# Kernel optimization log

Measured on AMD Instinct MI355X. Metric: run time of the kernel, lower is better.

Reference implementation:

```python
import jax, jax.numpy as jnp
import numpy as np

TEMPERATURE = 0.05
EPS = 1e-8  # torch.cosine_similarity eps


def setup_inputs() -> dict:
    key = jax.random.key(0)
    k1, k2 = jax.random.split(key)
    N, D = 8192, 256
    text_embeddings = jax.random.normal(k1, (N, D), dtype=jnp.float32)
    text_pos_embeddings = jax.random.normal(k2, (N, D), dtype=jnp.float32)
    return {"text_embeddings": text_embeddings, "text_pos_embeddings": text_pos_embeddings}


def reference(text_embeddings, text_pos_embeddings):
    # cosine similarity via normalize + single GEMM (same math as broadcasted
    # torch.cosine_similarity, which clamps norms at eps)
    a_norm = jnp.maximum(jnp.linalg.norm(text_embeddings, axis=-1, keepdims=True), EPS)
    b_norm = jnp.maximum(jnp.linalg.norm(text_pos_embeddings, axis=-1, keepdims=True), EPS)
    a = text_embeddings / a_norm  # [N, D]
    b = text_pos_embeddings / b_norm  # [N, D]
    sim = jnp.einsum("nd,md->nm", a, b) / TEMPERATURE  # [N, N]
    # cross-entropy with labels = arange(N): mean over rows of -log_softmax diag
    logp = jax.nn.log_softmax(sim, axis=-1)
    loss = -jnp.mean(jnp.diagonal(logp))
    return loss
```

## Files before the change

### kernel.cpp

```cpp
#include <hip/hip_runtime.h>
#include <hip/hip_bf16.h>
#include <math.h>

#define DIM 256

typedef float f32x4 __attribute__((ext_vector_type(4)));
typedef int   i32x8 __attribute__((ext_vector_type(8)));

__constant__ const float kTempInvLog2e = 20.0f * 1.4426950408889634f;
#define LN2 0.6931471805599453f
#define EPS_NORM 1e-8f
#define SCALE_ONE 0x7F7F7F7Fu

static __device__ inline unsigned f2fp8x4(float4 v, float s) {
    int r = 0;
    r = __builtin_amdgcn_cvt_pk_fp8_f32(v.x * s, v.y * s, r, false);
    r = __builtin_amdgcn_cvt_pk_fp8_f32(v.z * s, v.w * s, r, true);
    return (unsigned)r;
}

static __device__ inline i32x8 ld_frag32(const void* p0, const void* p1) {
    uint4 a = *(const uint4*)p0;
    uint4 b = *(const uint4*)p1;
    i32x8 v;
    v[0] = a.x; v[1] = a.y; v[2] = a.z; v[3] = a.w;
    v[4] = b.x; v[5] = b.y; v[6] = b.z; v[7] = b.w;
    return v;
}

__global__ __launch_bounds__(256) void normpack_kernel(
    const float* __restrict__ A, const float* __restrict__ B,
    unsigned char* __restrict__ Apk, unsigned char* __restrict__ Bpk,
    float* __restrict__ diag, float* __restrict__ rowsum,
    unsigned* __restrict__ counter, int n)
{
    __shared__ uint4 lA[256];
    __shared__ uint4 lB[256];
    const int t = threadIdx.x;
    const int rl = t >> 4;
    const int c16 = t & 15;
    const int r = blockIdx.x * 16 + rl;

    if (blockIdx.x == 0 && t == 0) counter[0] = 0;

    const float4* pa = (const float4*)(A + (size_t)r * DIM + c16 * 16);
    const float4* pb = (const float4*)(B + (size_t)r * DIM + c16 * 16);
    float4 a0 = pa[0], a1 = pa[1], a2 = pa[2], a3 = pa[3];
    float4 b0 = pb[0], b1 = pb[1], b2 = pb[2], b3 = pb[3];

    float ssa = a0.x*a0.x + a0.y*a0.y + a0.z*a0.z + a0.w*a0.w
              + a1.x*a1.x + a1.y*a1.y + a1.z*a1.z + a1.w*a1.w
              + a2.x*a2.x + a2.y*a2.y + a2.z*a2.z + a2.w*a2.w
              + a3.x*a3.x + a3.y*a3.y + a3.z*a3.z + a3.w*a3.w;
    float ssb = b0.x*b0.x + b0.y*b0.y + b0.z*b0.z + b0.w*b0.w
              + b1.x*b1.x + b1.y*b1.y + b1.z*b1.z + b1.w*b1.w
              + b2.x*b2.x + b2.y*b2.y + b2.z*b2.z + b2.w*b2.w
              + b3.x*b3.x + b3.y*b3.y + b3.z*b3.z + b3.w*b3.w;
    float dd  = a0.x*b0.x + a0.y*b0.y + a0.z*b0.z + a0.w*b0.w
              + a1.x*b1.x + a1.y*b1.y + a1.z*b1.z + a1.w*b1.w
              + a2.x*b2.x + a2.y*b2.y + a2.z*b2.z + a2.w*b2.w
              + a3.x*b3.x + a3.y*b3.y + a3.z*b3.z + a3.w*b3.w;
#pragma unroll
    for (int m = 1; m < 16; m <<= 1) {
        ssa += __shfl_xor(ssa, m, 64);
        ssb += __shfl_xor(ssb, m, 64);
        dd  += __shfl_xor(dd, m, 64);
    }
    float na = fmaxf(sqrtf(ssa), EPS_NORM);
    float nb = fmaxf(sqrtf(ssb), EPS_NORM);
    float sa = kTempInvLog2e / na;
    float sb = 1.0f / nb;
    if (c16 == 0) {
        diag[r] = dd / (na * nb) * kTempInvLog2e;
        rowsum[r] = 0.0f;
    }

    const int u = ((c16 >> 3) << 7) + ((c16 & 1) << 6) + rl + ((c16 & 7) >> 1) * 16;
    uint4 ga, gb;
    ga.x = f2fp8x4(a0, sa); ga.y = f2fp8x4(a1, sa);
    ga.z = f2fp8x4(a2, sa); ga.w = f2fp8x4(a3, sa);
    gb.x = f2fp8x4(b0, sb); gb.y = f2fp8x4(b1, sb);
    gb.z = f2fp8x4(b2, sb); gb.w = f2fp8x4(b3, sb);
    lA[u] = ga; lB[u] = gb;
    __syncthreads();

    ((uint4*)Apk)[(size_t)blockIdx.x * 256 + t] = lA[t];
    ((uint4*)Bpk)[(size_t)blockIdx.x * 256 + t] = lB[t];
}

static __device__ inline void async_copy16(const void* g, void* l) {
    __builtin_amdgcn_global_load_lds(
        (const __attribute__((address_space(1))) unsigned int*)g,
        (__attribute__((address_space(3))) unsigned int*)l, 16, 0, 0);
}

__global__ __launch_bounds__(256, 2) void gemm_lse_kernel(
    const unsigned char* __restrict__ Apk, const unsigned char* __restrict__ Bpk,
    float* __restrict__ rowsum, const float* __restrict__ diag,
    unsigned* __restrict__ counter, float* __restrict__ out, int n)
{
    __shared__ char ldsbuf[16384];
    const int t = threadIdx.x;
    const int lane = t & 63;
    const int w = t >> 6;
    const int c = lane & 15;
    const int q = lane >> 4;

    const int i = blockIdx.x;
    const int split = ((i & 7) << 1) | ((i >> 3) & 1);
    const int rowblk = i >> 4;
    const int rowbase = rowblk * 256 + w * 64;

    i32x8 afrag[4][2];
#pragma unroll
    for (int m = 0; m < 4; ++m) {
        const int AT = rowblk * 16 + w * 4 + m;
#pragma unroll
        for (int kc = 0; kc < 2; ++kc) {
            const char* base = (const char*)Apk + ((size_t)AT * 2 + kc) * 2048 + lane * 16;
            afrag[m][kc] = ld_frag32(base, base + 1024);
        }
    }
#pragma unroll
    for (int m = 0; m < 4; ++m)
#pragma unroll
        for (int kc = 0; kc < 2; ++kc)
            asm volatile("" : "+v"(afrag[m][kc]));

    float sums[16];
#pragma unroll
    for (int s = 0; s < 16; ++s) sums[s] = 0.0f;

    const char* bbase = (const char*)Bpk + (size_t)split * 32 * 4096;
    const int niter = 16;

    {
        const char* src = bbase + w * 2048 + (size_t)lane * 16;
        char* dst = ldsbuf + w * 2048;
        async_copy16(src, dst);
        async_copy16(src + 1024, dst + 1024);
    }
    __syncthreads();

    for (int it = 0; it < niter; ++it) {
        const int cur = it & 1;
        if (it + 1 < niter) {
            const char* src = bbase + (size_t)(it + 1) * 8192 + w * 2048 + (size_t)lane * 16;
            char* dst = ldsbuf + (cur ^ 1) * 8192 + w * 2048;
            async_copy16(src, dst);
            async_copy16(src + 1024, dst + 1024);
        }

        f32x4 acc[4][2];
#pragma unroll
        for (int m = 0; m < 4; ++m)
#pragma unroll
            for (int nc = 0; nc < 2; ++nc)
                acc[m][nc] = (f32x4){0.f, 0.f, 0.f, 0.f};

        const char* lb = ldsbuf + cur * 8192 + (size_t)lane * 16;
#pragma unroll
        for (int nc = 0; nc < 2; ++nc) {
#pragma unroll
            for (int kc = 0; kc < 2; ++kc) {
                const char* p = lb + nc * 4096 + kc * 2048;
                i32x8 bfrag = ld_frag32(p, p + 1024);
#pragma unroll
                for (int m = 0; m < 4; ++m)
                    acc[m][nc] = __builtin_amdgcn_mfma_scale_f32_16x16x128_f8f6f4(
                        afrag[m][kc], bfrag, acc[m][nc],
                        0, 0,
                        0, SCALE_ONE,
                        0, SCALE_ONE);
            }
        }

#pragma unroll
        for (int m = 0; m < 4; ++m)
#pragma unroll
            for (int nc = 0; nc < 2; ++nc)
#pragma unroll
                for (int r = 0; r < 4; ++r)
                    sums[m * 4 + r] += __builtin_amdgcn_exp2f(acc[m][nc][r]);

        __syncthreads();
    }

#pragma unroll
    for (int s = 0; s < 16; ++s) {
        float v = sums[s];
        v += __shfl_xor(v, 1, 64);
        v += __shfl_xor(v, 2, 64);
        v += __shfl_xor(v, 4, 64);
        v += __shfl_xor(v, 8, 64);
        sums[s] = v;
    }
    if (c == 0) {
#pragma unroll
        for (int m = 0; m < 4; ++m)
#pragma unroll
            for (int r = 0; r < 4; ++r)
                atomicAdd(&rowsum[rowbase + m * 16 + q * 4 + r], sums[m * 4 + r]);
    }

    __syncthreads();
    __shared__ unsigned lastFlag;
    if (t == 0) {
        __threadfence();
        lastFlag = (__hip_atomic_fetch_add(counter, 1u, __ATOMIC_ACQ_REL,
                                           __HIP_MEMORY_SCOPE_AGENT)
                    == gridDim.x - 1) ? 1u : 0u;
    }
    __syncthreads();
    if (lastFlag) {
        float local = 0.0f;
        for (int row = t; row < n; row += 256) {
            float rs = __hip_atomic_load(&rowsum[row], __ATOMIC_RELAXED,
                                         __HIP_MEMORY_SCOPE_AGENT);
            local += log2f(rs) - diag[row];
        }
#pragma unroll
        for (int m = 1; m < 64; m <<= 1)
            local += __shfl_xor(local, m, 64);
        float* red = (float*)ldsbuf;
        if ((t & 63) == 0) red[t >> 6] = local;
        __syncthreads();
        if (t == 0) out[0] = (red[0] + red[1] + red[2] + red[3]) * (LN2 / (float)n);
    }
}

extern "C" void kernel_launch(void* const* d_in, const int* in_sizes, int n_in,
                              void* d_out, int out_size, void* d_ws, size_t ws_size,
                              hipStream_t stream) {
    const int n = in_sizes[0] / DIM;
    const float* A = (const float*)d_in[0];
    const float* B = (const float*)d_in[1];
    float* out = (float*)d_out;

    unsigned char* Apk = (unsigned char*)d_ws;
    unsigned char* Bpk = Apk + (size_t)n * DIM;
    float* rowsum = (float*)(Bpk + (size_t)n * DIM);
    float* diag = rowsum + n;
    unsigned* counter = (unsigned*)(diag + n);

    normpack_kernel<<<n / 16, 256, 0, stream>>>(A, B, Apk, Bpk, diag, rowsum, counter, n);

    gemm_lse_kernel<<<(n / 256) * 16, 256, 0, stream>>>(Apk, Bpk, rowsum, diag, counter, out, n);
}
```

Measured before the change: 108.4 us.

## Load B fragments directly from global into registers with register double-buffering

Drops the LDS staging of B tiles (async global_load_lds plus per-iteration __syncthreads) and instead has each wave load its B fragments straight from global memory into two register buffers, ping-ponged across a fully unrolled loop. Each wave now reads the whole B tile itself instead of sharing one LDS copy across the block's four waves. This removes the block-wide barriers and LDS round-trips, but raises global/L2 traffic and register pressure, which may affect occupancy at 2 blocks per CU.

Result: no change. 108.0 us (-0.4%).

```diff
diff --git a/kernel.cpp b/kernel.cpp
--- a/kernel.cpp
+++ b/kernel.cpp
@@ -1,5 +1,4 @@
 #include <hip/hip_runtime.h>
-#include <hip/hip_bf16.h>
 #include <math.h>
 
 #define DIM 256
@@ -19,9 +18,7 @@
     return (unsigned)r;
 }
 
-static __device__ inline i32x8 ld_frag32(const void* p0, const void* p1) {
-    uint4 a = *(const uint4*)p0;
-    uint4 b = *(const uint4*)p1;
+static __device__ inline i32x8 mk_frag(uint4 a, uint4 b) {
     i32x8 v;
     v[0] = a.x; v[1] = a.y; v[2] = a.z; v[3] = a.w;
     v[4] = b.x; v[5] = b.y; v[6] = b.z; v[7] = b.w;
@@ -88,18 +85,11 @@
     ((uint4*)Bpk)[(size_t)blockIdx.x * 256 + t] = lB[t];
 }
 
-static __device__ inline void async_copy16(const void* g, void* l) {
-    __builtin_amdgcn_global_load_lds(
-        (const __attribute__((address_space(1))) unsigned int*)g,
-        (__attribute__((address_space(3))) unsigned int*)l, 16, 0, 0);
-}
-
 __global__ __launch_bounds__(256, 2) void gemm_lse_kernel(
     const unsigned char* __restrict__ Apk, const unsigned char* __restrict__ Bpk,
     float* __restrict__ rowsum, const float* __restrict__ diag,
     unsigned* __restrict__ counter, float* __restrict__ out, int n)
 {
-    __shared__ char ldsbuf[16384];
     const int t = threadIdx.x;
     const int lane = t & 63;
     const int w = t >> 6;
@@ -118,7 +108,7 @@
 #pragma unroll
         for (int kc = 0; kc < 2; ++kc) {
             const char* base = (const char*)Apk + ((size_t)AT * 2 + kc) * 2048 + lane * 16;
-            afrag[m][kc] = ld_frag32(base, base + 1024);
+            afrag[m][kc] = mk_frag(*(const uint4*)base, *(const uint4*)(base + 1024));
         }
     }
 #pragma unroll
@@ -131,60 +121,43 @@
 #pragma unroll
     for (int s = 0; s < 16; ++s) sums[s] = 0.0f;
 
-    const char* bbase = (const char*)Bpk + (size_t)split * 32 * 4096;
-    const int niter = 16;
-
-    {
-        const char* src = bbase + w * 2048 + (size_t)lane * 16;
-        char* dst = ldsbuf + w * 2048;
-        async_copy16(src, dst);
-        async_copy16(src + 1024, dst + 1024);
-    }
-    __syncthreads();
-
-    for (int it = 0; it < niter; ++it) {
-        const int cur = it & 1;
-        if (it + 1 < niter) {
-            const char* src = bbase + (size_t)(it + 1) * 8192 + w * 2048 + (size_t)lane * 16;
-            char* dst = ldsbuf + (cur ^ 1) * 8192 + w * 2048;
-            async_copy16(src, dst);
-            async_copy16(src + 1024, dst + 1024);
-        }
-
-        f32x4 acc[4][2];
-#pragma unroll
-        for (int m = 0; m < 4; ++m)
-#pragma unroll
-            for (int nc = 0; nc < 2; ++nc)
-                acc[m][nc] = (f32x4){0.f, 0.f, 0.f, 0.f};
-
-        const char* lb = ldsbuf + cur * 8192 + (size_t)lane * 16;
-#pragma unroll
-        for (int nc = 0; nc < 2; ++nc) {
-#pragma unroll
-            for (int kc = 0; kc < 2; ++kc) {
-                const char* p = lb + nc * 4096 + kc * 2048;
-                i32x8 bfrag = ld_frag32(p, p + 1024);
-#pragma unroll
-                for (int m = 0; m < 4; ++m)
-                    acc[m][nc] = __builtin_amdgcn_mfma_scale_f32_16x16x128_f8f6f4(
-                        afrag[m][kc], bfrag, acc[m][nc],
-                        0, 0,
-                        0, SCALE_ONE,
-                        0, SCALE_ONE);
-            }
-        }
-
-#pragma unroll
-        for (int m = 0; m < 4; ++m)
-#pragma unroll
-            for (int nc = 0; nc < 2; ++nc)
-#pragma unroll
-                for (int r = 0; r < 4; ++r)
-                    sums[m * 4 + r] += __builtin_amdgcn_exp2f(acc[m][nc][r]);
-
-        __syncthreads();
-    }
+    const char* bb = (const char*)Bpk + (size_t)split * 32 * 4096 + (size_t)lane * 16;
+
+#define LOADT(BUF, IT) do {                                                  \
+    _Pragma("unroll") for (int j = 0; j < 8; ++j)                            \
+        BUF[j] = *(const uint4*)(bb + (IT) * 8192 + j * 1024);               \
+} while (0)
+
+#define STEP(BUF) do {                                                       \
+    f32x4 acc[4][2];                                                         \
+    _Pragma("unroll") for (int m = 0; m < 4; ++m)                            \
+        _Pragma("unroll") for (int nc = 0; nc < 2; ++nc)                     \
+            acc[m][nc] = (f32x4){0.f, 0.f, 0.f, 0.f};                        \
+    _Pragma("unroll") for (int nc = 0; nc < 2; ++nc)                         \
+        _Pragma("unroll") for (int kc = 0; kc < 2; ++kc) {                   \
+            i32x8 bf = mk_frag(BUF[nc * 4 + kc * 2], BUF[nc * 4 + kc * 2 + 1]); \
+            _Pragma("unroll") for (int m = 0; m < 4; ++m)                    \
+                acc[m][nc] = __builtin_amdgcn_mfma_scale_f32_16x16x128_f8f6f4( \
+                    afrag[m][kc], bf, acc[m][nc],                            \
+                    0, 0, 0, SCALE_ONE, 0, SCALE_ONE);                       \
+        }                                                                    \
+    _Pragma("unroll") for (int m = 0; m < 4; ++m)                            \
+        _Pragma("unroll") for (int nc = 0; nc < 2; ++nc)                     \
+            _Pragma("unroll") for (int r = 0; r < 4; ++r)                    \
+                sums[m * 4 + r] += __builtin_amdgcn_exp2f(acc[m][nc][r]);    \
+} while (0)
+
+    uint4 bufA[8], bufB[8];
+    LOADT(bufA, 0);
+#pragma unroll
+    for (int ip = 0; ip < 8; ++ip) {
+        LOADT(bufB, 2 * ip + 1);
+        STEP(bufA);
+        if (2 * ip + 2 < 16) LOADT(bufA, 2 * ip + 2);
+        STEP(bufB);
+    }
+#undef LOADT
+#undef STEP
 
 #pragma unroll
     for (int s = 0; s < 16; ++s) {
@@ -205,6 +178,7 @@
 
     __syncthreads();
     __shared__ unsigned lastFlag;
+    __shared__ float red[4];
     if (t == 0) {
         __threadfence();
         lastFlag = (__hip_atomic_fetch_add(counter, 1u, __ATOMIC_ACQ_REL,
@@ -222,7 +196,6 @@
 #pragma unroll
         for (int m = 1; m < 64; m <<= 1)
             local += __shfl_xor(local, m, 64);
-        float* red = (float*)ldsbuf;
         if ((t & 63) == 0) red[t >> 6] = local;
         __syncthreads();
         if (t == 0) out[0] = (red[0] + red[1] + red[2] + red[3]) * (LN2 / (float)n);
```
